# Performance work log

Measured on AMD Instinct MI355X. Metric: run time of the kernel, lower is better.

## Reference

```python
import jax, jax.numpy as jnp
import numpy as np

DIM = 256
GROUPS = 32
EPS = 1e-6


def setup_inputs() -> dict:
    key = jax.random.key(0)
    ks = jax.random.split(key, 7)
    B, C, H, W = 4, DIM, 64, 64
    s = 1.0 / np.sqrt(C)
    return {
        "x": jax.random.normal(ks[0], (B, C, H, W), dtype=jnp.float32),
        "gamma": jnp.ones((C,), dtype=jnp.float32),
        "beta": jnp.zeros((C,), dtype=jnp.float32),
        "w_qkv": jax.random.normal(ks[1], (3 * C, C), dtype=jnp.float32) * s,
        "b_qkv": jnp.zeros((3 * C,), dtype=jnp.float32),
        "w_proj": jax.random.normal(ks[2], (C, C), dtype=jnp.float32) * s,
        "b_proj": jnp.zeros((C,), dtype=jnp.float32),
    }


def reference(x, gamma, beta, w_qkv, b_qkv, w_proj, b_proj):
    B, C, H, W = x.shape
    N = H * W
    scale = jnp.asarray(C, x.dtype) ** 0.5

    # GroupNorm(32, C, eps=1e-6, affine)
    h = x.reshape(B, GROUPS, C // GROUPS, N)
    mu = h.mean(axis=(2, 3), keepdims=True)
    var = h.var(axis=(2, 3), keepdims=True)
    h = (h - mu) * jax.lax.rsqrt(var + EPS)
    h = h.reshape(B, C, N) * gamma[None, :, None] + beta[None, :, None]

    # 1x1 conv QKV == channel matmul
    qkv = jnp.einsum('oc,bcn->bon', w_qkv, h) + b_qkv[None, :, None]  # (B,3C,N)
    qkv = qkv.reshape(B, 3, C, N)
    q = qkv[:, 0].transpose(0, 2, 1)  # (B,N,C)
    k = qkv[:, 1].transpose(0, 2, 1)
    v = qkv[:, 2].transpose(0, 2, 1)

    attn = jnp.einsum('bqc,bkc->bqk', q, k) / scale  # (B,N,N)
    attn = jax.nn.softmax(attn, axis=-1)
    out = jnp.einsum('bqk,bkc->bqc', attn, v)  # (B,N,C)

    out = out.transpose(0, 2, 1)  # (B,C,N)
    out = jnp.einsum('oc,bcn->bon', w_proj, out) + b_proj[None, :, None]
    return x + out.reshape(B, C, H, W)
```

## Files before the change

### kernel.cpp

```cpp
#include <hip/hip_runtime.h>
#include <stdint.h>

#define DIM 256
#define NPOS 4096
#define NB 4
#define GROUPS 32

typedef __attribute__((ext_vector_type(8))) short short8;
typedef __attribute__((ext_vector_type(4))) short short4v;
typedef __attribute__((ext_vector_type(4))) float f32x4;
typedef __attribute__((ext_vector_type(16))) float f32x16;
typedef __attribute__((ext_vector_type(2))) unsigned int u32x2;
typedef __attribute__((ext_vector_type(4))) unsigned int u32x4;

__device__ __forceinline__ short f2b(float f) {
  unsigned u = __float_as_uint(f);
  unsigned r = (u + 0x7fffu + ((u >> 16) & 1u)) >> 16;
  return (short)r;
}

__device__ __forceinline__ void gl16(const short* g, char* lds) {
  __builtin_amdgcn_global_load_lds((const __attribute__((address_space(1))) void*)g,
                                   (__attribute__((address_space(3))) void*)lds, 16, 0, 0);
}

__global__ void k_convert_w(const float* __restrict__ wq, const float* __restrict__ wp,
                            short* __restrict__ wqb, short* __restrict__ wpb) {
  int i = blockIdx.x * 256 + threadIdx.x;
  if (i < 768 * 256) wqb[i] = f2b(wq[i]);
  if (i < 256 * 256) wpb[i] = f2b(wp[i]);
}

__global__ void k_gn_stats(const float* __restrict__ x, float* __restrict__ stats) {
  int bg = blockIdx.x;
  const float4* b4 = (const float4*)(x + (size_t)bg * 8 * NPOS);
  float s = 0.f, ss = 0.f;
  for (int i = threadIdx.x; i < 8192; i += 256) {
    float4 v = b4[i];
    s  += v.x + v.y + v.z + v.w;
    ss += v.x * v.x + v.y * v.y + v.z * v.z + v.w * v.w;
  }
  #pragma unroll
  for (int m = 1; m < 64; m <<= 1) { s += __shfl_xor(s, m, 64); ss += __shfl_xor(ss, m, 64); }
  __shared__ float red[8];
  int wid = threadIdx.x >> 6;
  if ((threadIdx.x & 63) == 0) { red[wid * 2] = s; red[wid * 2 + 1] = ss; }
  __syncthreads();
  if (threadIdx.x == 0) {
    float S = red[0] + red[2] + red[4] + red[6];
    float SS = red[1] + red[3] + red[5] + red[7];
    float mean = S / 32768.f;
    float var = SS / 32768.f - mean * mean;
    stats[bg * 2] = mean;
    stats[bg * 2 + 1] = rsqrtf(var + 1e-6f);
  }
}

__global__ void k_gn_apply(const float* __restrict__ x, const float* __restrict__ stats,
                           const float* __restrict__ gamma, const float* __restrict__ beta,
                           short* __restrict__ ht) {
  int ct = blockIdx.x, nt = blockIdx.y, b = blockIdx.z;
  int c0 = ct * 64, n0 = nt * 64;
  __shared__ short lt[64 * 72];
  int t = threadIdx.x;
  #pragma unroll
  for (int p = 0; p < 4; ++p) {
    int row = (t >> 4) + p * 16;
    int colb = (t & 15) * 4;
    int c = c0 + row;
    float mean = stats[(b * GROUPS + (c >> 3)) * 2];
    float rstd = stats[(b * GROUPS + (c >> 3)) * 2 + 1];
    float ga = gamma[c], be = beta[c];
    float4 v = *(const float4*)(x + ((size_t)(b * DIM + c)) * NPOS + n0 + colb);
    short4v o;
    o.x = f2b((v.x - mean) * rstd * ga + be);
    o.y = f2b((v.y - mean) * rstd * ga + be);
    o.z = f2b((v.z - mean) * rstd * ga + be);
    o.w = f2b((v.w - mean) * rstd * ga + be);
    *(short4v*)&lt[row * 72 + colb] = o;
  }
  __syncthreads();
  #pragma unroll
  for (int p = 0; p < 2; ++p) {
    int nr = (t >> 3) + p * 32;
    int ch = t & 7;
    short8 o;
    #pragma unroll
    for (int j = 0; j < 8; ++j) o[j] = lt[(ch * 8 + j) * 72 + nr];
    *(short8*)(ht + ((size_t)(b * NPOS + n0 + nr)) * DIM + c0 + ch * 8) = o;
  }
}

template <int MODE>
__launch_bounds__(256, 2)
__global__ void k_gemm(const short* __restrict__ A, const short* __restrict__ Bm,
                       const float* __restrict__ bias,
                       short* __restrict__ qb, short* __restrict__ kb, short* __restrict__ vtb,
                       const float* __restrict__ resid, float* __restrict__ outf) {
  const int K = 256;
  int b = blockIdx.z;
  int m0 = blockIdx.x * 128, n0 = blockIdx.y * 128;
  const short* Ap = (MODE == 0) ? A + (size_t)b * NPOS * K : A;
  const short* Bp = (MODE == 0) ? Bm : Bm + (size_t)b * NPOS * K;

  __shared__ short As[128 * 64], Bs[128 * 64];
  int t = threadIdx.x;
  int lane = t & 63, wid = t >> 6;
  int wm = wid >> 1, wn = wid & 1;
  f32x4 acc[4][4] = {};

  for (int kt = 0; kt < 4; ++kt) {
    int k0 = kt * 64;
    short8 av[4], bv[4];
    #pragma unroll
    for (int p = 0; p < 4; ++p) {
      int ci = t + p * 256;
      int row = ci >> 3, ch = ci & 7;
      av[p] = *(const short8*)(Ap + (size_t)(m0 + row) * K + k0 + ch * 8);
      bv[p] = *(const short8*)(Bp + (size_t)(n0 + row) * K + k0 + ch * 8);
    }
    __syncthreads();
    #pragma unroll
    for (int p = 0; p < 4; ++p) {
      int ci = t + p * 256;
      int row = ci >> 3, ch = ci & 7;
      int off = (row * 128 + ch * 16) ^ ((row & 7) << 4);
      *(short8*)((char*)As + off) = av[p];
      *(short8*)((char*)Bs + off) = bv[p];
    }
    __syncthreads();
    #pragma unroll
    for (int ks = 0; ks < 2; ++ks) {
      short8 af[4], bf[4];
      int inner = ks * 64 + (lane >> 4) * 16;
      #pragma unroll
      for (int mi = 0; mi < 4; ++mi) {
        int row = wm * 64 + mi * 16 + (lane & 15);
        af[mi] = *(short8*)((char*)As + ((row * 128 + inner) ^ ((row & 7) << 4)));
      }
      #pragma unroll
      for (int ni = 0; ni < 4; ++ni) {
        int row = wn * 64 + ni * 16 + (lane & 15);
        bf[ni] = *(short8*)((char*)Bs + ((row * 128 + inner) ^ ((row & 7) << 4)));
      }
      #pragma unroll
      for (int mi = 0; mi < 4; ++mi)
        #pragma unroll
        for (int ni = 0; ni < 4; ++ni)
          acc[mi][ni] = __builtin_amdgcn_mfma_f32_16x16x32_bf16(af[mi], bf[ni], acc[mi][ni], 0, 0, 0);
    }
  }

  #pragma unroll
  for (int mi = 0; mi < 4; ++mi)
    #pragma unroll
    for (int ni = 0; ni < 4; ++ni) {
      int gcol = n0 + wn * 64 + ni * 16 + (lane & 15);
      #pragma unroll
      for (int r = 0; r < 4; ++r) {
        int grow = m0 + wm * 64 + mi * 16 + (lane >> 4) * 4 + r;
        if (MODE == 0) {
          float v = acc[mi][ni][r] + bias[gcol];
          short h = f2b(v);
          if (gcol < 256)       qb[((size_t)b * NPOS + grow) * DIM + gcol] = h;
          else if (gcol < 512)  kb[((size_t)b * NPOS + grow) * DIM + gcol - 256] = h;
          else                  vtb[((size_t)b * DIM + gcol - 512) * NPOS + grow] = h;
        } else {
          float v = acc[mi][ni][r] + bias[grow];
          size_t idx = ((size_t)b * DIM + grow) * NPOS + gcol;
          outf[idx] = v + resid[idx];
        }
      }
    }
}

__launch_bounds__(512, 2)
__global__ void k_flash(const short* __restrict__ qb, const short* __restrict__ kb,
                        const short* __restrict__ vtb, short* __restrict__ ob) {
  __shared__ __align__(16) char smem[131072];

  int i = blockIdx.x;
  int xcd = i & 7, slot = i >> 3;
  int b = xcd >> 1;
  int bx = slot * 2 + (xcd & 1);
  int q0 = bx * 64;

  int t = threadIdx.x, lane = t & 63, wid = t >> 6;
  int q = lane & 31, hi = lane >> 5;
  int qs = wid & 1, h = (wid >> 1) & 1, ds = wid >> 2;

  const short* kbB = kb + (size_t)b * NPOS * DIM;
  const short* vbB = vtb + (size_t)b * DIM * NPOS;

  short8 qf[16];
  {
    int qrow = q0 + qs * 32 + q;
    const short* qp = qb + ((size_t)b * NPOS + qrow) * DIM + hi * 8;
    #pragma unroll
    for (int s = 0; s < 16; ++s) {
      short8 v = *(const short8*)(qp + s * 16);
      #pragma unroll
      for (int j = 0; j < 8; ++j) {
        float f = __uint_as_float(((unsigned)(unsigned short)v[j]) << 16) * 0.0625f;
        v[j] = f2b(f);
      }
      qf[s] = v;
    }
  }

  const short* srcK[4];
  const short* srcV[4];
  unsigned dstK[4], dstV[4];
  #pragma unroll
  for (int j = 0; j < 4; ++j) {
    int c = wid * 4 + j;
    int ch = c >> 4;
    int kr = (c & 15) * 2 + (lane >> 5);
    int kcol = ((lane & 31) * 16) ^ ((kr & 7) << 4);
    srcK[j] = kbB + (size_t)(ch * 2048 + kr) * DIM + (kcol >> 1);
    int dr = (c & 15) * 16 + (lane >> 2);
    int vcol = ((lane & 3) * 16) ^ ((dr & 6) << 3);
    srcV[j] = vbB + (size_t)dr * NPOS + ch * 2048 + (vcol >> 1);
    dstK[j] = (unsigned)c * 1024u;
    dstV[j] = 65536u + (unsigned)c * 1024u;
  }

  f32x16 oacc[4] = {};
  float m = -1e30f, l = 0.f;

  const int NIT = 64;
  int buf = 0;
  #pragma unroll
  for (int j = 0; j < 4; ++j) {
    gl16(srcK[j], smem + dstK[j]);
    gl16(srcV[j], smem + dstV[j]);
  }
  __syncthreads();

  const unsigned kx = (unsigned)((q & 7) << 4);
  const unsigned vx = (unsigned)((q & 6) << 3);

  for (int it = 0; it < NIT; ++it) {
    if (it + 1 < NIT) {
      size_t ko = (size_t)(it + 1) * 32 * DIM;
      int vo = (it + 1) * 32;
      unsigned nb = (unsigned)(buf ^ 1) * 32768u;
      #pragma unroll
      for (int j = 0; j < 4; ++j) {
        gl16(srcK[j] + ko, smem + nb + dstK[j]);
        gl16(srcV[j] + vo, smem + nb + dstV[j]);
      }
    }

    const char* kl = smem + (unsigned)buf * 32768u + h * 16384u;
    const char* vl = smem + 65536u + (unsigned)buf * 32768u + h * 16384u;
    f32x16 sacc = {};
    #pragma unroll
    for (int s = 0; s < 16; ++s) {
      short8 kf = *(const short8*)(kl + q * 512u + ((s * 32u + hi * 16u) ^ kx));
      sacc = __builtin_amdgcn_mfma_f32_32x32x16_bf16(kf, qf[s], sacc, 0, 0, 0);
    }

    float mx = sacc[0];
    #pragma unroll
    for (int r = 1; r < 16; ++r) mx = fmaxf(mx, sacc[r]);
    mx = fmaxf(mx, __shfl_xor(mx, 32, 64));
    if (!__all(mx <= m + 8.f)) {
      float mn = fmaxf(m, mx);
      float al = __expf(m - mn);
      m = mn; l *= al;
      #pragma unroll
      for (int dt = 0; dt < 4; ++dt)
        #pragma unroll
        for (int r = 0; r < 16; ++r) oacc[dt][r] *= al;
    }
    float p_[16];
    float ts = 0.f;
    #pragma unroll
    for (int r = 0; r < 16; ++r) { p_[r] = __expf(sacc[r] - m); ts += p_[r]; }
    ts += __shfl_xor(ts, 32, 64);
    l += ts;

    unsigned w0, w1, w2, w3, w4, w5, w6, w7;
    asm("v_cvt_pk_bf16_f32 %0, %1, %2" : "=v"(w0) : "v"(p_[0]),  "v"(p_[1]));
    asm("v_cvt_pk_bf16_f32 %0, %1, %2" : "=v"(w1) : "v"(p_[2]),  "v"(p_[3]));
    asm("v_cvt_pk_bf16_f32 %0, %1, %2" : "=v"(w2) : "v"(p_[4]),  "v"(p_[5]));
    asm("v_cvt_pk_bf16_f32 %0, %1, %2" : "=v"(w3) : "v"(p_[6]),  "v"(p_[7]));
    asm("v_cvt_pk_bf16_f32 %0, %1, %2" : "=v"(w4) : "v"(p_[8]),  "v"(p_[9]));
    asm("v_cvt_pk_bf16_f32 %0, %1, %2" : "=v"(w5) : "v"(p_[10]), "v"(p_[11]));
    asm("v_cvt_pk_bf16_f32 %0, %1, %2" : "=v"(w6) : "v"(p_[12]), "v"(p_[13]));
    asm("v_cvt_pk_bf16_f32 %0, %1, %2" : "=v"(w7) : "v"(p_[14]), "v"(p_[15]));
    asm("v_permlane32_swap_b32 %0, %1" : "+v"(w0), "+v"(w2));
    asm("v_permlane32_swap_b32 %0, %1" : "+v"(w1), "+v"(w3));
    asm("v_permlane32_swap_b32 %0, %1" : "+v"(w4), "+v"(w6));
    asm("v_permlane32_swap_b32 %0, %1" : "+v"(w5), "+v"(w7));
    short8 pf0 = __builtin_bit_cast(short8, (u32x4){w0, w1, w2, w3});
    short8 pf1 = __builtin_bit_cast(short8, (u32x4){w4, w5, w6, w7});

    #pragma unroll
    for (int dtl = 0; dtl < 4; ++dtl) {
      unsigned vrow = ((ds * 4 + dtl) * 32u + q) * 64u;
      short8 vf0 = *(const short8*)(vl + vrow + ((hi * 16u) ^ vx));
      short8 vf1 = *(const short8*)(vl + vrow + ((32u + hi * 16u) ^ vx));
      oacc[dtl] = __builtin_amdgcn_mfma_f32_32x32x16_bf16(vf0, pf0, oacc[dtl], 0, 0, 0);
      oacc[dtl] = __builtin_amdgcn_mfma_f32_32x32x16_bf16(vf1, pf1, oacc[dtl], 0, 0, 0);
    }
    __syncthreads();
    buf ^= 1;
  }

  float* lmm = (float*)(smem + 100352);
  float* lml = lmm + 128;
  if (ds == 0 && lane < 32) { lmm[(qs * 2 + h) * 32 + q] = m; lml[(qs * 2 + h) * 32 + q] = l; }
  __syncthreads();
  float mo = lmm[(qs * 2 + (h ^ 1)) * 32 + q];
  float lo = lml[(qs * 2 + (h ^ 1)) * 32 + q];
  float M = fmaxf(m, mo);
  float al = __expf(m - M);
  float Lf = l * al + lo * __expf(mo - M);
  float iL = 1.f / Lf;

  float* sc32 = (float*)smem;
  short* sc16 = (short*)(smem + 66560);
  if (h == 0) {
    #pragma unroll
    for (int dtl = 0; dtl < 4; ++dtl)
      #pragma unroll
      for (int r = 0; r < 16; ++r) {
        int d = (ds * 4 + dtl) * 32 + (r & 3) + 8 * (r >> 2) + 4 * hi;
        sc32[qs * 8224 + q * 257 + d] = oacc[dtl][r] * al;
      }
  }
  __syncthreads();
  if (h == 1) {
    #pragma unroll
    for (int dtl = 0; dtl < 4; ++dtl)
      #pragma unroll
      for (int r = 0; r < 16; ++r) {
        int d = (ds * 4 + dtl) * 32 + (r & 3) + 8 * (r >> 2) + 4 * hi;
        float v = (sc32[qs * 8224 + q * 257 + d] + oacc[dtl][r] * al) * iL;
        sc16[qs * 8256 + q * 258 + d] = f2b(v);
      }
  }
  __syncthreads();
  {
    int row = t >> 3;
    const short* src = sc16 + (row >> 5) * 8256 + (row & 31) * 258 + (t & 7) * 32;
    short* dst = ob + ((size_t)b * NPOS + q0 + row) * DIM + (t & 7) * 32;
    #pragma unroll
    for (int j = 0; j < 4; ++j)
      *(short8*)(dst + j * 8) = *(const short8*)(src + j * 8);
  }
}

extern "C" void kernel_launch(void* const* d_in, const int* in_sizes, int n_in,
                              void* d_out, int out_size, void* d_ws, size_t ws_size,
                              hipStream_t stream) {
  const float* x     = (const float*)d_in[0];
  const float* gamma = (const float*)d_in[1];
  const float* beta  = (const float*)d_in[2];
  const float* wqkv  = (const float*)d_in[3];
  const float* bqkv  = (const float*)d_in[4];
  const float* wproj = (const float*)d_in[5];
  const float* bproj = (const float*)d_in[6];
  float* out = (float*)d_out;

  char* ws = (char*)d_ws;
  float* stats = (float*)ws;
  short* wqb = (short*)(ws + 1024);
  short* wpb = (short*)(ws + 1024 + 393216);
  size_t off = 1024 + 393216 + 131072;
  const size_t SZ = (size_t)NB * NPOS * DIM * sizeof(short);
  short* ht   = (short*)(ws + off); off += SZ;
  short* qbuf = (short*)(ws + off); off += SZ;
  short* kbuf = (short*)(ws + off); off += SZ;
  short* vtb  = (short*)(ws + off); off += SZ;
  short* obuf = ht;

  k_convert_w<<<768, 256, 0, stream>>>(wqkv, wproj, wqb, wpb);
  k_gn_stats<<<128, 256, 0, stream>>>(x, stats);
  k_gn_apply<<<dim3(4, 64, NB), 256, 0, stream>>>(x, stats, gamma, beta, ht);
  k_gemm<0><<<dim3(32, 6, NB), 256, 0, stream>>>(ht, wqb, bqkv, qbuf, kbuf, vtb, nullptr, nullptr);
  k_flash<<<dim3(256), 512, 0, stream>>>(qbuf, kbuf, vtb, obuf);
  k_gemm<1><<<dim3(2, 32, NB), 256, 0, stream>>>(wpb, obuf, bproj, nullptr, nullptr, nullptr, x, out);
}
```

Before: 182.5 us.

## Restructure flash kernel to 32-query blocks without split-KV merge, use exp2

The flash attention kernel changes from 512-thread blocks covering 64 queries, with the key range split across two wave halves and merged through shared memory, to 256-thread blocks covering 32 queries that each walk all 4096 keys. This removes the cross-half max/sum merge and the fp32 staging pass, halves LDS use to 64KB, and doubles the grid to 512 blocks. The softmax now uses exp2f with log2(e) folded into the query prescale, and the rescale threshold is widened to match. Each block now loads K/V tiles for only 32 queries, which doubles K/V traffic per query, and the loop runs twice as many iterations.

```diff
diff --git a/kernel.cpp b/kernel.cpp
--- a/kernel.cpp
+++ b/kernel.cpp
@@ -174,34 +174,34 @@
     }
 }
 
-__launch_bounds__(512, 2)
+__launch_bounds__(256, 2)
 __global__ void k_flash(const short* __restrict__ qb, const short* __restrict__ kb,
                         const short* __restrict__ vtb, short* __restrict__ ob) {
-  __shared__ __align__(16) char smem[131072];
+  __shared__ __align__(16) char smem[65536];
 
   int i = blockIdx.x;
   int xcd = i & 7, slot = i >> 3;
   int b = xcd >> 1;
   int bx = slot * 2 + (xcd & 1);
-  int q0 = bx * 64;
+  int q0 = bx * 32;
 
   int t = threadIdx.x, lane = t & 63, wid = t >> 6;
   int q = lane & 31, hi = lane >> 5;
-  int qs = wid & 1, h = (wid >> 1) & 1, ds = wid >> 2;
+  int ds = wid;
 
   const short* kbB = kb + (size_t)b * NPOS * DIM;
   const short* vbB = vtb + (size_t)b * DIM * NPOS;
 
   short8 qf[16];
   {
-    int qrow = q0 + qs * 32 + q;
+    int qrow = q0 + q;
     const short* qp = qb + ((size_t)b * NPOS + qrow) * DIM + hi * 8;
     #pragma unroll
     for (int s = 0; s < 16; ++s) {
       short8 v = *(const short8*)(qp + s * 16);
       #pragma unroll
       for (int j = 0; j < 8; ++j) {
-        float f = __uint_as_float(((unsigned)(unsigned short)v[j]) << 16) * 0.0625f;
+        float f = __uint_as_float(((unsigned)(unsigned short)v[j]) << 16) * 0.090168440f;
         v[j] = f2b(f);
       }
       qf[s] = v;
@@ -214,21 +214,20 @@
   #pragma unroll
   for (int j = 0; j < 4; ++j) {
     int c = wid * 4 + j;
-    int ch = c >> 4;
-    int kr = (c & 15) * 2 + (lane >> 5);
+    int kr = c * 2 + (lane >> 5);
     int kcol = ((lane & 31) * 16) ^ ((kr & 7) << 4);
-    srcK[j] = kbB + (size_t)(ch * 2048 + kr) * DIM + (kcol >> 1);
-    int dr = (c & 15) * 16 + (lane >> 2);
+    srcK[j] = kbB + (size_t)kr * DIM + (kcol >> 1);
+    int dr = c * 16 + (lane >> 2);
     int vcol = ((lane & 3) * 16) ^ ((dr & 6) << 3);
-    srcV[j] = vbB + (size_t)dr * NPOS + ch * 2048 + (vcol >> 1);
+    srcV[j] = vbB + (size_t)dr * NPOS + (vcol >> 1);
     dstK[j] = (unsigned)c * 1024u;
-    dstV[j] = 65536u + (unsigned)c * 1024u;
-  }
-
-  f32x16 oacc[4] = {};
+    dstV[j] = 32768u + (unsigned)c * 1024u;
+  }
+
+  f32x16 oacc[2] = {};
   float m = -1e30f, l = 0.f;
 
-  const int NIT = 64;
+  const int NIT = 128;
   int buf = 0;
   #pragma unroll
   for (int j = 0; j < 4; ++j) {
@@ -244,7 +243,7 @@
     if (it + 1 < NIT) {
       size_t ko = (size_t)(it + 1) * 32 * DIM;
       int vo = (it + 1) * 32;
-      unsigned nb = (unsigned)(buf ^ 1) * 32768u;
+      unsigned nb = (unsigned)(buf ^ 1) * 16384u;
       #pragma unroll
       for (int j = 0; j < 4; ++j) {
         gl16(srcK[j] + ko, smem + nb + dstK[j]);
@@ -252,8 +251,8 @@
       }
     }
 
-    const char* kl = smem + (unsigned)buf * 32768u + h * 16384u;
-    const char* vl = smem + 65536u + (unsigned)buf * 32768u + h * 16384u;
+    const char* kl = smem + (unsigned)buf * 16384u;
+    const char* vl = smem + 32768u + (unsigned)buf * 16384u;
     f32x16 sacc = {};
     #pragma unroll
     for (int s = 0; s < 16; ++s) {
@@ -265,19 +264,19 @@
     #pragma unroll
     for (int r = 1; r < 16; ++r) mx = fmaxf(mx, sacc[r]);
     mx = fmaxf(mx, __shfl_xor(mx, 32, 64));
-    if (!__all(mx <= m + 8.f)) {
+    if (!__all(mx <= m + 11.5f)) {
       float mn = fmaxf(m, mx);
-      float al = __expf(m - mn);
+      float al = exp2f(m - mn);
       m = mn; l *= al;
       #pragma unroll
-      for (int dt = 0; dt < 4; ++dt)
+      for (int dt = 0; dt < 2; ++dt)
         #pragma unroll
         for (int r = 0; r < 16; ++r) oacc[dt][r] *= al;
     }
     float p_[16];
     float ts = 0.f;
     #pragma unroll
-    for (int r = 0; r < 16; ++r) { p_[r] = __expf(sacc[r] - m); ts += p_[r]; }
+    for (int r = 0; r < 16; ++r) { p_[r] = exp2f(sacc[r] - m); ts += p_[r]; }
     ts += __shfl_xor(ts, 32, 64);
     l += ts;
 
@@ -298,8 +297,8 @@
     short8 pf1 = __builtin_bit_cast(short8, (u32x4){w4, w5, w6, w7});
 
     #pragma unroll
-    for (int dtl = 0; dtl < 4; ++dtl) {
-      unsigned vrow = ((ds * 4 + dtl) * 32u + q) * 64u;
+    for (int dtl = 0; dtl < 2; ++dtl) {
+      unsigned vrow = ((ds * 2 + dtl) * 32u + q) * 64u;
       short8 vf0 = *(const short8*)(vl + vrow + ((hi * 16u) ^ vx));
       short8 vf1 = *(const short8*)(vl + vrow + ((32u + hi * 16u) ^ vx));
       oacc[dtl] = __builtin_amdgcn_mfma_f32_32x32x16_bf16(vf0, pf0, oacc[dtl], 0, 0, 0);
@@ -309,43 +308,19 @@
     buf ^= 1;
   }
 
-  float* lmm = (float*)(smem + 100352);
-  float* lml = lmm + 128;
-  if (ds == 0 && lane < 32) { lmm[(qs * 2 + h) * 32 + q] = m; lml[(qs * 2 + h) * 32 + q] = l; }
-  __syncthreads();
-  float mo = lmm[(qs * 2 + (h ^ 1)) * 32 + q];
-  float lo = lml[(qs * 2 + (h ^ 1)) * 32 + q];
-  float M = fmaxf(m, mo);
-  float al = __expf(m - M);
-  float Lf = l * al + lo * __expf(mo - M);
-  float iL = 1.f / Lf;
-
-  float* sc32 = (float*)smem;
-  short* sc16 = (short*)(smem + 66560);
-  if (h == 0) {
-    #pragma unroll
-    for (int dtl = 0; dtl < 4; ++dtl)
-      #pragma unroll
-      for (int r = 0; r < 16; ++r) {
-        int d = (ds * 4 + dtl) * 32 + (r & 3) + 8 * (r >> 2) + 4 * hi;
-        sc32[qs * 8224 + q * 257 + d] = oacc[dtl][r] * al;
-      }
-  }
-  __syncthreads();
-  if (h == 1) {
-    #pragma unroll
-    for (int dtl = 0; dtl < 4; ++dtl)
-      #pragma unroll
-      for (int r = 0; r < 16; ++r) {
-        int d = (ds * 4 + dtl) * 32 + (r & 3) + 8 * (r >> 2) + 4 * hi;
-        float v = (sc32[qs * 8224 + q * 257 + d] + oacc[dtl][r] * al) * iL;
-        sc16[qs * 8256 + q * 258 + d] = f2b(v);
-      }
-  }
+  float iL = 1.f / l;
+  short* sc16 = (short*)smem;
+  #pragma unroll
+  for (int dtl = 0; dtl < 2; ++dtl)
+    #pragma unroll
+    for (int r = 0; r < 16; ++r) {
+      int d = (ds * 2 + dtl) * 32 + (r & 3) + 8 * (r >> 2) + 4 * hi;
+      sc16[q * 258 + d] = f2b(oacc[dtl][r] * iL);
+    }
   __syncthreads();
   {
     int row = t >> 3;
-    const short* src = sc16 + (row >> 5) * 8256 + (row & 31) * 258 + (t & 7) * 32;
+    const short* src = sc16 + row * 258 + (t & 7) * 32;
     short* dst = ob + ((size_t)b * NPOS + q0 + row) * DIM + (t & 7) * 32;
     #pragma unroll
     for (int j = 0; j < 4; ++j)
@@ -381,6 +356,6 @@
   k_gn_stats<<<128, 256, 0, stream>>>(x, stats);
   k_gn_apply<<<dim3(4, 64, NB), 256, 0, stream>>>(x, stats, gamma, beta, ht);
   k_gemm<0><<<dim3(32, 6, NB), 256, 0, stream>>>(ht, wqb, bqkv, qbuf, kbuf, vtb, nullptr, nullptr);
-  k_flash<<<dim3(256), 512, 0, stream>>>(qbuf, kbuf, vtb, obuf);
+  k_flash<<<dim3(512), 256, 0, stream>>>(qbuf, kbuf, vtb, obuf);
   k_gemm<1><<<dim3(2, 32, NB), 256, 0, stream>>>(wpb, obuf, bproj, nullptr, nullptr, nullptr, x, out);
 }
```

After: 275.7 us. 1.51x slower.
